# Kernel tuning notes

Hardware: AMD Instinct MI355X
Metric: run time of the kernel (lower is better)

Reference implementation:

```python
import jax, jax.numpy as jnp
import numpy as np
import math

B, NX, NY = 4, 64, 64
IN_DIM, OUT_DIM = 3, 3
DIM, DEPTH, HEADS, DH, FF_MULT = 192, 6, 8, 64, 4
INNER = HEADS * DH              # 512
FF = DIM * FF_MULT              # 768
M = int(DH * math.log(DH))      # 266 random features (performer default)
GROUPS = 8
LATENT_STEPS = 1
EPS_SN, EPS_K, EPS_GN = 1e-5, 1e-4, 1e-5


def setup_inputs() -> dict:
    rng = np.random.default_rng(0)
    f = lambda *s: jnp.asarray(rng.standard_normal(s).astype(np.float32) * 0.02)
    # unitary forward operator (SVD-whitened in torch == orthogonal matrix)
    Q, _ = np.linalg.qr(rng.standard_normal((DIM, DIM)).astype(np.float32))
    return {
        "x": jnp.asarray(rng.standard_normal((B, NX, NY, IN_DIM)).astype(np.float32)),
        "to_in_w": f(DIM, IN_DIM), "to_in_b": f(DIM),
        "pos_emb": f(1, NX * NY, DIM),
        "proj": jnp.asarray(rng.standard_normal((DEPTH, M, DH)).astype(np.float32)),
        "sn_attn_g": jnp.ones((DEPTH,), jnp.float32),
        "wq": f(DEPTH, INNER, DIM), "wk": f(DEPTH, INNER, DIM), "wv": f(DEPTH, INNER, DIM),
        "wo": f(DEPTH, DIM, INNER), "bo": f(DEPTH, DIM),
        "sn_ff_g": jnp.ones((DEPTH,), jnp.float32),
        "w1": f(DEPTH, FF, DIM), "b1": f(DEPTH, FF),
        "w2": f(DEPTH, DIM, FF), "b2": f(DEPTH, DIM),
        "expand_w": f(DIM, DIM),
        "fwd_w": jnp.asarray(Q.astype(np.float32)),
        "dec_lin_w": f(DIM, DIM), "dec_lin_b": f(DIM),
        "gn_g": jnp.ones((DIM,), jnp.float32), "gn_b": jnp.zeros((DIM,), jnp.float32),
        "c9_w": f(DIM, DIM // GROUPS, 9, 9), "c9_b": f(DIM),
        "c7_w": f(DIM // 2, DIM // GROUPS, 7, 7), "c7_b": f(DIM // 2),
        "c5_w": f(DIM // 4, (DIM // 2) // GROUPS, 5, 5), "c5_b": f(DIM // 4),
        "c1_w": f(OUT_DIM, DIM // 4, 1, 1), "c1_b": f(OUT_DIM),
        "latent_steps": LATENT_STEPS,
    }


def _scalenorm(x, g):
    n = jnp.linalg.norm(x, axis=-1, keepdims=True) * (x.shape[-1] ** -0.5)
    return x / jnp.maximum(n, EPS_SN) * g


def _softmax_features(data, proj, is_query):
    # data: [b,h,n,d]; proj: [m,d] -> FAVOR+ softmax-kernel features [b,h,n,m]
    dn = data.shape[-1] ** -0.25
    ratio = proj.shape[0] ** -0.5
    dd = jnp.einsum('bhnd,md->bhnm', data * dn, proj)
    diag = 0.5 * jnp.sum(data * data, -1) * (dn * dn)  # [b,h,n]
    if is_query:
        mx = jnp.max(dd, axis=-1, keepdims=True)
    else:
        mx = jnp.max(dd, axis=(-1, -2), keepdims=True)
    return ratio * (jnp.exp(dd - diag[..., None] - mx) + EPS_K)


def _attn(x, proj, wq, wk, wv, wo, bo):
    b, n, _ = x.shape
    split = lambda t: t.reshape(b, n, HEADS, DH).transpose(0, 2, 1, 3)
    q = split(x @ wq.T); k = split(x @ wk.T); v = split(x @ wv.T)
    qp = _softmax_features(q, proj, True)
    kp = _softmax_features(k, proj, False)
    context = jnp.einsum('bhnm,bhnd->bhmd', kp, v)            # [b,h,m,d]
    denom = jnp.einsum('bhnm,bhm->bhn', qp, kp.sum(2))
    out = jnp.einsum('bhnm,bhmd->bhnd', qp, context) / denom[..., None]
    out = out.transpose(0, 2, 1, 3).reshape(b, n, INNER)
    return out @ wo.T + bo


def _circ_conv(x, w, b, groups):
    p = w.shape[-1] // 2
    x = jnp.pad(x, ((0, 0), (0, 0), (p, p), (p, p)), mode='wrap')
    y = jax.lax.conv_general_dilated(x, w, (1, 1), 'VALID',
        dimension_numbers=('NCHW', 'OIHW', 'NCHW'), feature_group_count=groups)
    return y + b[None, :, None, None]


def _group_norm(x, g, b):
    B_, C, H, W = x.shape
    xg = x.reshape(B_, GROUPS, C // GROUPS, H, W)
    mu = xg.mean((2, 3, 4), keepdims=True)
    var = xg.var((2, 3, 4), keepdims=True)
    xn = ((xg - mu) * jax.lax.rsqrt(var + EPS_GN)).reshape(B_, C, H, W)
    return xn * g[None, :, None, None] + b[None, :, None, None]


def reference(x, to_in_w, to_in_b, pos_emb, proj, sn_attn_g, wq, wk, wv, wo, bo,
              sn_ff_g, w1, b1, w2, b2, expand_w, fwd_w, dec_lin_w, dec_lin_b,
              gn_g, gn_b, c9_w, c9_b, c7_w, c7_b, c5_w, c5_b, c1_w, c1_b, latent_steps):
    b, nx, ny, _ = x.shape
    h = x @ to_in_w.T + to_in_b                       # [b,nx,ny,dim]
    h = h.reshape(b, nx * ny, DIM) + pos_emb[:, :nx * ny]
    for i in range(DEPTH):                             # Performer: prenorm attn + prenorm FF
        h = h + _attn(_scalenorm(h, sn_attn_g[i]), proj[i], wq[i], wk[i], wv[i], wo[i], bo[i])
        hn = _scalenorm(h, sn_ff_g[i])
        h = h + (jax.nn.gelu(hn @ w1[i].T + b1[i], approximate=False) @ w2[i].T + b2[i])
    h = h.reshape(b, nx, ny, DIM) @ expand_w.T        # expand_latent (no bias)
    u, us = h, []
    for _ in range(latent_steps):
        u = u @ fwd_w.T                               # unitary forward operator
        us.append(u)
    u = jnp.concatenate(us, 0)                        # [(b*t), nx, ny, c]
    y = u @ dec_lin_w.T + dec_lin_b
    y = y.transpose(0, 3, 1, 2)                       # NCHW
    y = _group_norm(y, gn_g, gn_b)
    y = jax.nn.gelu(_circ_conv(y, c9_w, c9_b, GROUPS), approximate=False)
    y = jax.nn.gelu(_circ_conv(y, c7_w, c7_b, GROUPS), approximate=False)
    y = jax.nn.gelu(_circ_conv(y, c5_w, c5_b, GROUPS), approximate=False)
    y = jax.lax.conv_general_dilated(y, c1_w, (1, 1), 'VALID',
        dimension_numbers=('NCHW', 'OIHW', 'NCHW')) + c1_b[None, :, None, None]
    # einops '(b t) c nx ny -> b t nx ny c'
    y = y.reshape(b, latent_steps, OUT_DIM, nx, ny).transpose(0, 1, 3, 4, 2)
    return y
```

## Files before the change

### kernel.cpp

```cpp
#include <hip/hip_runtime.h>
#include <cmath>

#define NB      4
#define NTOK    4096
#define BNTOK   16384
#define CDIM    192
#define CINNER  512
#define NHEADS  8
#define DHEAD   64
#define CFF     768
#define MFEAT   266
#define NDEPTH  6

#define DN      0.35355339059327373f
#define RATIO   0.06131393394849658f

typedef unsigned short u16;
typedef __attribute__((ext_vector_type(8))) short s16x8;
typedef __attribute__((ext_vector_type(8))) u16  u16x8;
typedef __attribute__((ext_vector_type(4))) float f32x4;

#define OFF_H    0ull
#define OFF_HN   3145728ull
#define OFF_Q    6291456ull
#define OFF_K    14680064ull
#define OFF_V    23068672ull
#define OFF_BIG  31457280ull
#define OFF_PJ   44040192ull
#define OFF_CTXT 44163072ull
#define OFF_KMAX 47368192ull
#define OFF_GNP  47368448ull
#define OFF_GNS  47369472ull
#define OFF_WHI  47370240ull
#define OFF_WLO  49489920ull
#define WOFF_QKV 0ull
#define WOFF_WO  1769472ull
#define WOFF_W1  2359296ull
#define WOFF_W2  3244032ull
#define WOFF_EXP 4128768ull
#define WOFF_FWD 4165632ull
#define WOFF_DEC 4202496ull

#define PJL      20480
#define CTXTN    819200

__device__ __forceinline__ float gelu_f(float x) {
    return 0.5f * x * (1.0f + erff(x * 0.7071067811865476f));
}
__device__ __forceinline__ unsigned f2ord(float f) {
    int i = __float_as_int(f);
    return (i >= 0) ? ((unsigned)i | 0x80000000u) : (unsigned)(~i);
}
__device__ __forceinline__ float ord2f(unsigned u) {
    int i = (u & 0x80000000u) ? (int)(u & 0x7fffffffu) : ~(int)u;
    return __int_as_float(i);
}
__device__ __forceinline__ void split_bf16(float a, u16& h, u16& l) {
    unsigned ua = __float_as_uint(a);
    unsigned rh = (ua + 0x7FFFu + ((ua >> 16) & 1u)) >> 16;
    h = (u16)rh;
    float hf = __uint_as_float(rh << 16);
    float lo = a - hf;
    unsigned ul = __float_as_uint(lo);
    unsigned rl = (ul + 0x7FFFu + ((ul >> 16) & 1u)) >> 16;
    l = (u16)rl;
}
__device__ __forceinline__ u16 hi_bf16(float a) {
    unsigned ua = __float_as_uint(a);
    return (u16)((ua + 0x7FFFu + ((ua >> 16) & 1u)) >> 16);
}

__global__ __launch_bounds__(256) void cvt_qkv(const float* __restrict__ wq,
    const float* __restrict__ wk, const float* __restrict__ wv,
    u16* __restrict__ hi, u16* __restrict__ lo)
{
    int idx = blockIdx.x * 256 + threadIdx.x;
    int l = idx / 294912, rem = idx - l * 294912;
    int r = rem / 192, c = rem - r * 192;
    float v;
    if (r < 512)       v = wq[((size_t)l * 512 + r) * 192 + c];
    else if (r < 1024) v = wk[((size_t)l * 512 + (r - 512)) * 192 + c];
    else               v = wv[((size_t)l * 512 + (r - 1024)) * 192 + c];
    u16 h, lw; split_bf16(v, h, lw);
    hi[idx] = h; lo[idx] = lw;
}

__global__ __launch_bounds__(256) void cvt_w(const float* __restrict__ src,
    u16* __restrict__ hi, u16* __restrict__ lo, int n)
{
    int idx = blockIdx.x * 256 + threadIdx.x;
    if (idx < n) {
        u16 h, l; split_bf16(src[idx], h, l);
        hi[idx] = h; lo[idx] = l;
    }
}

__global__ __launch_bounds__(256) void cvt_dec(const float* __restrict__ e,
    const float* __restrict__ f, const float* __restrict__ d,
    u16* __restrict__ hi, u16* __restrict__ lo)
{
    int idx = blockIdx.x * 256 + threadIdx.x;
    if (idx >= 110592) return;
    int which = idx / 36864, rem = idx - which * 36864;
    float v = (which == 0) ? e[rem] : (which == 1) ? f[rem] : d[rem];
    u16 h, l; split_bf16(v, h, l);
    hi[idx] = h; lo[idx] = l;
}

__global__ __launch_bounds__(256) void cvt_pj(const float* __restrict__ proj,
    u16* __restrict__ hi, u16* __restrict__ lo)
{
    int idx = blockIdx.x * 256 + threadIdx.x;
    int l = idx / PJL, rem = idx - l * PJL;
    int m = rem >> 6, k = rem & 63;
    float v = (m < MFEAT) ? proj[(size_t)l * MFEAT * DHEAD + m * 64 + k] : 0.f;
    u16 h, lw; split_bf16(v, h, lw);
    hi[idx] = h; lo[idx] = lw;
}

__global__ __launch_bounds__(256) void input_embed(const float* __restrict__ x,
    const float* __restrict__ w, const float* __restrict__ bvec,
    const float* __restrict__ pos, float* __restrict__ h)
{
    int idx = blockIdx.x * 256 + threadIdx.x;
    int row = idx / CDIM, c = idx - row * CDIM;
    int p = row & (NTOK - 1);
    const float* xr = x + (size_t)row * 3;
    h[idx] = xr[0]*w[c*3+0] + xr[1]*w[c*3+1] + xr[2]*w[c*3+2] + bvec[c] + pos[(size_t)p*CDIM + c];
}

__global__ __launch_bounds__(256) void rownorm_kernel(const float* __restrict__ in,
    float* __restrict__ sv, const float* __restrict__ gptr, int gidx)
{
    int wv = threadIdx.x >> 6, lane = threadIdx.x & 63;
    int row = blockIdx.x * 4 + wv;
    const float* p = in + (size_t)row * CDIM;
    float x0 = p[lane], x1 = p[lane + 64], x2 = p[lane + 128];
    float ss = x0*x0 + x1*x1 + x2*x2;
    #pragma unroll
    for (int off = 32; off; off >>= 1) ss += __shfl_xor(ss, off);
    if (lane == 0) {
        float g = gptr[gidx];
        float n = sqrtf(ss * (1.0f / 192.0f));
        sv[row] = g / fmaxf(n, 1e-5f);
    }
}

#define LP 40
__global__ __launch_bounds__(256) void gemm_mfma(const float* __restrict__ A,
    const float* __restrict__ ascale,
    const u16* __restrict__ Bhi, const u16* __restrict__ Blo,
    const float* __restrict__ bias, const float* __restrict__ resid,
    float* __restrict__ C, int M, int N, int K, int epi)
{
    __shared__ u16 a_hi[128 * LP], a_lo[128 * LP], b_hi[128 * LP], b_lo[128 * LP];
    const int tid = threadIdx.x;
    const int n0 = blockIdx.x * 128, m0 = blockIdx.y * 128;
    const int wave = tid >> 6, lane = tid & 63;
    const int wr = wave >> 1, wc = wave & 1;
    const int fr = lane & 15, q = lane >> 4;
    const bool wactive = (n0 + wc * 64) < N;
    f32x4 acc[4][4];
    #pragma unroll
    for (int i = 0; i < 4; ++i)
        #pragma unroll
        for (int j = 0; j < 4; ++j) { acc[i][j][0]=0.f; acc[i][j][1]=0.f; acc[i][j][2]=0.f; acc[i][j][3]=0.f; }

    const int srow = tid >> 1, sc0 = (tid & 1) * 16;
    const float* aptr = A + (size_t)(m0 + srow) * K + sc0;
    const float as = ascale ? ascale[m0 + srow] : 1.0f;
    const bool bval = (n0 + srow) < N;
    const u16* bhp = Bhi + (size_t)(n0 + srow) * K + sc0;
    const u16* blp = Blo + (size_t)(n0 + srow) * K + sc0;
    const int soff = srow * LP + sc0;
    const int aoffb = (wr * 64 + fr) * LP + q * 8;
    const int boffb = (wc * 64 + fr) * LP + q * 8;

    for (int kc = 0; kc < K; kc += 32) {
        float4 f0 = *(const float4*)(aptr + kc);
        float4 f1 = *(const float4*)(aptr + kc + 4);
        float4 f2 = *(const float4*)(aptr + kc + 8);
        float4 f3 = *(const float4*)(aptr + kc + 12);
        u16x8 h0, l0, h1, l1;
        {
            float v[16] = {f0.x,f0.y,f0.z,f0.w, f1.x,f1.y,f1.z,f1.w,
                           f2.x,f2.y,f2.z,f2.w, f3.x,f3.y,f3.z,f3.w};
            u16 hh[16], ll[16];
            #pragma unroll
            for (int i = 0; i < 16; ++i) { float sv = v[i] * as; split_bf16(sv, hh[i], ll[i]); }
            #pragma unroll
            for (int i = 0; i < 8; ++i) { h0[i]=hh[i]; l0[i]=ll[i]; h1[i]=hh[8+i]; l1[i]=ll[8+i]; }
        }
        *(u16x8*)&a_hi[soff]     = h0;  *(u16x8*)&a_hi[soff + 8] = h1;
        *(u16x8*)&a_lo[soff]     = l0;  *(u16x8*)&a_lo[soff + 8] = l1;
        u16x8 bh0 = (u16x8)0, bh1 = (u16x8)0, bl0 = (u16x8)0, bl1 = (u16x8)0;
        if (bval) {
            bh0 = *(const u16x8*)(bhp + kc);  bh1 = *(const u16x8*)(bhp + kc + 8);
            bl0 = *(const u16x8*)(blp + kc);  bl1 = *(const u16x8*)(blp + kc + 8);
        }
        *(u16x8*)&b_hi[soff]     = bh0;  *(u16x8*)&b_hi[soff + 8] = bh1;
        *(u16x8*)&b_lo[soff]     = bl0;  *(u16x8*)&b_lo[soff + 8] = bl1;
        __syncthreads();
        if (wactive) {
            s16x8 Ah[4], Al[4], Bh[4], Bl[4];
            #pragma unroll
            for (int t = 0; t < 4; ++t) {
                Ah[t] = *(const s16x8*)&a_hi[aoffb + t * 16 * LP];
                Al[t] = *(const s16x8*)&a_lo[aoffb + t * 16 * LP];
                Bh[t] = *(const s16x8*)&b_hi[boffb + t * 16 * LP];
                Bl[t] = *(const s16x8*)&b_lo[boffb + t * 16 * LP];
            }
            #pragma unroll
            for (int i = 0; i < 4; ++i)
                #pragma unroll
                for (int j = 0; j < 4; ++j)
                    acc[i][j] = __builtin_amdgcn_mfma_f32_16x16x32_bf16(Ah[i], Bh[j], acc[i][j], 0, 0, 0);
            #pragma unroll
            for (int i = 0; i < 4; ++i)
                #pragma unroll
                for (int j = 0; j < 4; ++j)
                    acc[i][j] = __builtin_amdgcn_mfma_f32_16x16x32_bf16(Ah[i], Bl[j], acc[i][j], 0, 0, 0);
            #pragma unroll
            for (int i = 0; i < 4; ++i)
                #pragma unroll
                for (int j = 0; j < 4; ++j)
                    acc[i][j] = __builtin_amdgcn_mfma_f32_16x16x32_bf16(Al[i], Bh[j], acc[i][j], 0, 0, 0);
        }
        __syncthreads();
    }
    const int c0 = n0 + wc * 64;
    const int rowb = m0 + wr * 64;
    #pragma unroll
    for (int j = 0; j < 4; ++j) {
        int c = c0 + j * 16 + fr;
        if (c >= N) continue;
        float bb = (epi & 1) ? bias[c] : 0.f;
        float* cp;
        if (epi & 8) cp = C + (size_t)(c >> 9) * 8388608ull + (size_t)(c & 511);
        else         cp = C + c;
        const float* rp = (epi & 4) ? (resid + c) : nullptr;
        #pragma unroll
        for (int i = 0; i < 4; ++i) {
            #pragma unroll
            for (int r = 0; r < 4; ++r) {
                int row = rowb + i * 16 + q * 4 + r;
                float val = acc[i][j][r] + bb;
                if (epi & 2) val = gelu_f(val);
                if (epi & 4) val += rp[(size_t)row * N];
                size_t off = (epi & 8) ? (size_t)row * 512 : (size_t)row * N;
                cp[off] = val;
            }
        }
    }
}

__global__ void kmax_init(unsigned* kmaxu) {
    if (threadIdx.x < NDEPTH * 32) kmaxu[threadIdx.x] = 0u;
}

__global__ __launch_bounds__(256) void kmax2_kernel(const float* __restrict__ Km,
    const u16* __restrict__ pjh, unsigned* __restrict__ kmaxu)
{
    __shared__ __align__(16) u16 khi[64 * 72];
    __shared__ float wred[4];
    const int tid = threadIdx.x;
    const int nt = blockIdx.x, bh = blockIdx.y;
    const int b = bh >> 3, hh = bh & 7;
    const int wave = tid >> 6, lane = tid & 63;
    const int fr = lane & 15, quad = lane >> 4;
    float lm = -1e30f;
    const size_t kbase = ((size_t)b * NTOK) * CINNER + hh * DHEAD;
    for (int ch = 0; ch < 4; ++ch) {
        const int n0 = nt * 256 + ch * 64;
        __syncthreads();
        {
            int tok = tid >> 2, koff = (tid & 3) * 16;
            const float* kp = Km + kbase + (size_t)(n0 + tok) * CINNER + koff;
            u16 hh16[16];
            #pragma unroll
            for (int qd = 0; qd < 4; ++qd) {
                float4 f = *(const float4*)(kp + qd * 4);
                hh16[qd*4+0] = hi_bf16(f.x * DN); hh16[qd*4+1] = hi_bf16(f.y * DN);
                hh16[qd*4+2] = hi_bf16(f.z * DN); hh16[qd*4+3] = hi_bf16(f.w * DN);
            }
            u16x8 v0, v1;
            #pragma unroll
            for (int i = 0; i < 8; ++i) { v0[i] = hh16[i]; v1[i] = hh16[8+i]; }
            *(u16x8*)&khi[tok * 72 + koff] = v0;
            *(u16x8*)&khi[tok * 72 + koff + 8] = v1;
        }
        __syncthreads();
        int rowA = (wave * 16 + fr) * 72;
        s16x8 A0 = *(const s16x8*)&khi[rowA + quad * 8];
        s16x8 A1 = *(const s16x8*)&khi[rowA + 32 + quad * 8];
        for (int ct = 0; ct < 17; ++ct) {
            const u16* bp = pjh + (ct * 16 + fr) * 64 + quad * 8;
            s16x8 B0 = *(const s16x8*)bp;
            s16x8 B1 = *(const s16x8*)(bp + 32);
            f32x4 t; t[0]=0.f; t[1]=0.f; t[2]=0.f; t[3]=0.f;
            t = __builtin_amdgcn_mfma_f32_16x16x32_bf16(A0, B0, t, 0, 0, 0);
            t = __builtin_amdgcn_mfma_f32_16x16x32_bf16(A1, B1, t, 0, 0, 0);
            if (ct * 16 + fr < MFEAT) {
                #pragma unroll
                for (int r = 0; r < 4; ++r) lm = fmaxf(lm, t[r]);
            }
        }
    }
    #pragma unroll
    for (int off = 32; off; off >>= 1) lm = fmaxf(lm, __shfl_xor(lm, off));
    if (lane == 0) wred[wave] = lm;
    __syncthreads();
    if (tid == 0) {
        float m = fmaxf(fmaxf(wred[0], wred[1]), fmaxf(wred[2], wred[3]));
        atomicMax(kmaxu + bh, f2ord(m));
    }
}

__global__ __launch_bounds__(256) void ctx2_kernel(const float* __restrict__ Km,
    const float* __restrict__ Vm, const u16* __restrict__ pjh, const u16* __restrict__ pjl,
    const unsigned* __restrict__ kmaxu, float* __restrict__ part)
{
    __shared__ __align__(16) u16 khi[32 * 72], klo[32 * 72];
    __shared__ __align__(16) u16 vth[80 * 40], vtl[80 * 40];
    __shared__ __align__(16) u16 kph[4][16 * 40], kpl[4][16 * 40];
    __shared__ float diag[32];
    const int tid = threadIdx.x;
    const int bh = blockIdx.x, seg = blockIdx.y;
    const int b = bh >> 3, hh = bh & 7;
    const int wave = tid >> 6, lane = tid & 63;
    const int fr = lane & 15, quad = lane >> 4;
    const float kmx = ord2f(kmaxu[bh]);
    for (int i = tid; i < 16 * 40; i += 256) {
        int row = 64 + i / 40, col = i - (i / 40) * 40;
        vth[row * 40 + col] = (row == 64) ? (u16)0x3F80 : (u16)0;
        vtl[row * 40 + col] = 0;
    }
    f32x4 accv[5][5];
    #pragma unroll
    for (int i = 0; i < 5; ++i)
        #pragma unroll
        for (int j = 0; j < 5; ++j) { accv[i][j][0]=0.f; accv[i][j][1]=0.f; accv[i][j][2]=0.f; accv[i][j][3]=0.f; }
    const size_t rowbase = ((size_t)b * NTOK) * CINNER + hh * DHEAD;
    u16* sh = kph[wave];  u16* sl = kpl[wave];
    for (int nc = 0; nc < 16; ++nc) {
        const int n0 = seg * 512 + nc * 32;
        __syncthreads();
        {
            int tok = tid >> 3, koff = (tid & 7) * 8;
            const float* kp = Km + rowbase + (size_t)(n0 + tok) * CINNER + koff;
            float4 f0 = *(const float4*)kp;
            float4 f1 = *(const float4*)(kp + 4);
            float v[8] = {f0.x*DN, f0.y*DN, f0.z*DN, f0.w*DN, f1.x*DN, f1.y*DN, f1.z*DN, f1.w*DN};
            u16x8 hv, lv; float ps = 0.f;
            #pragma unroll
            for (int i = 0; i < 8; ++i) { u16 h, l; split_bf16(v[i], h, l); hv[i]=h; lv[i]=l; ps += v[i]*v[i]; }
            *(u16x8*)&khi[tok * 72 + koff] = hv;
            *(u16x8*)&klo[tok * 72 + koff] = lv;
            ps += __shfl_xor(ps, 1); ps += __shfl_xor(ps, 2); ps += __shfl_xor(ps, 4);
            if ((tid & 7) == 0) diag[tok] = 0.5f * ps;
            const float* vp = Vm + rowbase + (size_t)(n0 + tok) * CINNER + koff;
            float4 g0 = *(const float4*)vp;
            float4 g1 = *(const float4*)(vp + 4);
            float vv[8] = {g0.x, g0.y, g0.z, g0.w, g1.x, g1.y, g1.z, g1.w};
            #pragma unroll
            for (int i = 0; i < 8; ++i) {
                u16 h, l; split_bf16(vv[i], h, l);
                vth[(koff + i) * 40 + tok] = h;
                vtl[(koff + i) * 40 + tok] = l;
            }
        }
        __syncthreads();
        s16x8 Ah[2][2], Al[2][2];
        #pragma unroll
        for (int rt = 0; rt < 2; ++rt) {
            int rowA = (rt * 16 + fr) * 72;
            Ah[rt][0] = *(const s16x8*)&khi[rowA + quad * 8];
            Ah[rt][1] = *(const s16x8*)&khi[rowA + 32 + quad * 8];
            Al[rt][0] = *(const s16x8*)&klo[rowA + quad * 8];
            Al[rt][1] = *(const s16x8*)&klo[rowA + 32 + quad * 8];
        }
        for (int mc = 0; mc < 5; ++mc) {
            const int ct = mc * 4 + wave;
            const u16* bph = pjh + (ct * 16 + fr) * 64 + quad * 8;
            const u16* bpl = pjl + (ct * 16 + fr) * 64 + quad * 8;
            s16x8 B0h = *(const s16x8*)bph, B1h = *(const s16x8*)(bph + 32);
            s16x8 B0l = *(const s16x8*)bpl, B1l = *(const s16x8*)(bpl + 32);
            const bool valid = (ct * 16 + fr) < MFEAT;
            #pragma unroll
            for (int rt = 0; rt < 2; ++rt) {
                f32x4 dd; dd[0]=0.f; dd[1]=0.f; dd[2]=0.f; dd[3]=0.f;
                dd = __builtin_amdgcn_mfma_f32_16x16x32_bf16(Ah[rt][0], B0h, dd, 0, 0, 0);
                dd = __builtin_amdgcn_mfma_f32_16x16x32_bf16(Ah[rt][0], B0l, dd, 0, 0, 0);
                dd = __builtin_amdgcn_mfma_f32_16x16x32_bf16(Al[rt][0], B0h, dd, 0, 0, 0);
                dd = __builtin_amdgcn_mfma_f32_16x16x32_bf16(Ah[rt][1], B1h, dd, 0, 0, 0);
                dd = __builtin_amdgcn_mfma_f32_16x16x32_bf16(Ah[rt][1], B1l, dd, 0, 0, 0);
                dd = __builtin_amdgcn_mfma_f32_16x16x32_bf16(Al[rt][1], B1h, dd, 0, 0, 0);
                ushort4 ph, pl;
                #pragma unroll
                for (int r = 0; r < 4; ++r) {
                    float dgv = diag[rt * 16 + quad * 4 + r];
                    float val = valid ? RATIO * (expf(dd[r] - dgv - kmx) + 1e-4f) : 0.f;
                    u16 h, l; split_bf16(val, h, l);
                    (&ph.x)[r] = h; (&pl.x)[r] = l;
                }
                *(ushort4*)&sh[fr * 40 + rt * 16 + quad * 4] = ph;
                *(ushort4*)&sl[fr * 40 + rt * 16 + quad * 4] = pl;
            }
            s16x8 Bh = *(const s16x8*)&sh[fr * 40 + quad * 8];
            s16x8 Bl = *(const s16x8*)&sl[fr * 40 + quad * 8];
            #pragma unroll
            for (int rt2 = 0; rt2 < 5; ++rt2) {
                s16x8 Vh = *(const s16x8*)&vth[(rt2 * 16 + fr) * 40 + quad * 8];
                s16x8 Vl = *(const s16x8*)&vtl[(rt2 * 16 + fr) * 40 + quad * 8];
                accv[rt2][mc] = __builtin_amdgcn_mfma_f32_16x16x32_bf16(Vh, Bh, accv[rt2][mc], 0, 0, 0);
                accv[rt2][mc] = __builtin_amdgcn_mfma_f32_16x16x32_bf16(Vh, Bl, accv[rt2][mc], 0, 0, 0);
                accv[rt2][mc] = __builtin_amdgcn_mfma_f32_16x16x32_bf16(Vl, Bh, accv[rt2][mc], 0, 0, 0);
            }
        }
    }
    float* pb = part + ((size_t)(seg * 32 + bh)) * 80 * 320;
    #pragma unroll
    for (int rt2 = 0; rt2 < 5; ++rt2) {
        #pragma unroll
        for (int mc = 0; mc < 5; ++mc) {
            int ct = mc * 4 + wave;
            #pragma unroll
            for (int r = 0; r < 4; ++r)
                pb[(size_t)(rt2 * 16 + quad * 4 + r) * 320 + ct * 16 + fr] = accv[rt2][mc][r];
        }
    }
}

__global__ __launch_bounds__(256) void ctxt_reduce(const float* __restrict__ part,
    u16* __restrict__ cth, u16* __restrict__ ctl)
{
    int idx = blockIdx.x * 256 + threadIdx.x;
    float s = 0.f;
    #pragma unroll
    for (int sg = 0; sg < 8; ++sg) s += part[(size_t)sg * CTXTN + idx];
    u16 h, l; split_bf16(s, h, l);
    cth[idx] = h; ctl[idx] = l;
}

__global__ __launch_bounds__(256) void qside2_kernel(const float* __restrict__ Qm,
    const u16* __restrict__ pjh, const u16* __restrict__ pjl,
    const u16* __restrict__ cth, const u16* __restrict__ ctl,
    float* __restrict__ attn_out)
{
    __shared__ __align__(16) u16 qhi[64 * 72], qlo[64 * 72];
    __shared__ __align__(16) u16 slabh[4][16 * 72], slabl[4][16 * 72];
    __shared__ float diag[64];
    const int tid = threadIdx.x;
    const int nt = blockIdx.x, bh = blockIdx.y;
    const int b = bh >> 3, hh = bh & 7;
    const int wave = tid >> 6, lane = tid & 63;
    const int fr = lane & 15, quad = lane >> 4;
    const int n0 = nt * 64;
    {
        int tok = tid >> 2, koff = (tid & 3) * 16;
        const float* qp = Qm + ((size_t)(b * NTOK + n0 + tok)) * CINNER + hh * DHEAD + koff;
        float v[16]; float ps = 0.f;
        #pragma unroll
        for (int qd = 0; qd < 4; ++qd) {
            float4 f = *(const float4*)(qp + qd * 4);
            v[qd*4+0]=f.x*DN; v[qd*4+1]=f.y*DN; v[qd*4+2]=f.z*DN; v[qd*4+3]=f.w*DN;
        }
        u16x8 h0, l0, h1, l1;
        #pragma unroll
        for (int i = 0; i < 8; ++i) {
            u16 h, l; split_bf16(v[i], h, l); h0[i]=h; l0[i]=l;
            split_bf16(v[8+i], h, l); h1[i]=h; l1[i]=l;
        }
        #pragma unroll
        for (int i = 0; i < 16; ++i) ps += v[i]*v[i];
        *(u16x8*)&qhi[tok * 72 + koff] = h0;  *(u16x8*)&qhi[tok * 72 + koff + 8] = h1;
        *(u16x8*)&qlo[tok * 72 + koff] = l0;  *(u16x8*)&qlo[tok * 72 + koff + 8] = l1;
        ps += __shfl_xor(ps, 1); ps += __shfl_xor(ps, 2);
        if ((tid & 3) == 0) diag[tok] = 0.5f * ps;
    }
    __syncthreads();
    f32x4 dd[20];
    #pragma unroll
    for (int ct = 0; ct < 20; ++ct) { dd[ct][0]=0.f; dd[ct][1]=0.f; dd[ct][2]=0.f; dd[ct][3]=0.f; }
    {
        int rowA = (wave * 16 + fr) * 72;
        s16x8 A0h = *(const s16x8*)&qhi[rowA + quad * 8];
        s16x8 A1h = *(const s16x8*)&qhi[rowA + 32 + quad * 8];
        s16x8 A0l = *(const s16x8*)&qlo[rowA + quad * 8];
        s16x8 A1l = *(const s16x8*)&qlo[rowA + 32 + quad * 8];
        #pragma unroll
        for (int ct = 0; ct < 20; ++ct) {
            const u16* bph = pjh + (ct * 16 + fr) * 64 + quad * 8;
            const u16* bpl = pjl + (ct * 16 + fr) * 64 + quad * 8;
            s16x8 B0h = *(const s16x8*)bph, B1h = *(const s16x8*)(bph + 32);
            s16x8 B0l = *(const s16x8*)bpl, B1l = *(const s16x8*)(bpl + 32);
            dd[ct] = __builtin_amdgcn_mfma_f32_16x16x32_bf16(A0h, B0h, dd[ct], 0, 0, 0);
            dd[ct] = __builtin_amdgcn_mfma_f32_16x16x32_bf16(A0h, B0l, dd[ct], 0, 0, 0);
            dd[ct] = __builtin_amdgcn_mfma_f32_16x16x32_bf16(A0l, B0h, dd[ct], 0, 0, 0);
            dd[ct] = __builtin_amdgcn_mfma_f32_16x16x32_bf16(A1h, B1h, dd[ct], 0, 0, 0);
            dd[ct] = __builtin_amdgcn_mfma_f32_16x16x32_bf16(A1h, B1l, dd[ct], 0, 0, 0);
            dd[ct] = __builtin_amdgcn_mfma_f32_16x16x32_bf16(A1l, B1h, dd[ct], 0, 0, 0);
        }
    }
    float pm[4] = {-1e30f, -1e30f, -1e30f, -1e30f};
    #pragma unroll
    for (int ct = 0; ct < 20; ++ct) {
        if (ct * 16 + fr < MFEAT) {
            #pragma unroll
            for (int r = 0; r < 4; ++r) pm[r] = fmaxf(pm[r], dd[ct][r]);
        }
    }
    #pragma unroll
    for (int r = 0; r < 4; ++r) {
        pm[r] = fmaxf(pm[r], __shfl_xor(pm[r], 1));
        pm[r] = fmaxf(pm[r], __shfl_xor(pm[r], 2));
        pm[r] = fmaxf(pm[r], __shfl_xor(pm[r], 4));
        pm[r] = fmaxf(pm[r], __shfl_xor(pm[r], 8));
    }
    float dg[4];
    #pragma unroll
    for (int r = 0; r < 4; ++r) dg[r] = diag[wave * 16 + quad * 4 + r];
    #pragma unroll
    for (int ct = 0; ct < 20; ++ct) {
        bool valid = (ct * 16 + fr) < MFEAT;
        #pragma unroll
        for (int r = 0; r < 4; ++r)
            dd[ct][r] = valid ? RATIO * (expf(dd[ct][r] - dg[r] - pm[r]) + 1e-4f) : 0.f;
    }
    f32x4 acc[5];
    #pragma unroll
    for (int dt = 0; dt < 5; ++dt) { acc[dt][0]=0.f; acc[dt][1]=0.f; acc[dt][2]=0.f; acc[dt][3]=0.f; }
    u16* sh = slabh[wave];  u16* sl = slabl[wave];
    for (int mc = 0; mc < 5; ++mc) {
        #pragma unroll
        for (int c = 0; c < 4; ++c) {
            int ct = mc * 4 + c;
            #pragma unroll
            for (int r = 0; r < 4; ++r) {
                u16 h, l; split_bf16(dd[ct][r], h, l);
                int tok = quad * 4 + r;
                sh[tok * 72 + c * 16 + fr] = h;
                sl[tok * 72 + c * 16 + fr] = l;
            }
        }
        #pragma unroll
        for (int ks = 0; ks < 2; ++ks) {
            s16x8 Ah = *(const s16x8*)&sh[fr * 72 + ks * 32 + quad * 8];
            s16x8 Al = *(const s16x8*)&sl[fr * 72 + ks * 32 + quad * 8];
            #pragma unroll
            for (int dt = 0; dt < 5; ++dt) {
                const u16* bph = cth + ((size_t)bh * 80 + dt * 16 + fr) * 320 + mc * 64 + ks * 32 + quad * 8;
                const u16* bpl = ctl + ((size_t)bh * 80 + dt * 16 + fr) * 320 + mc * 64 + ks * 32 + quad * 8;
                s16x8 Bh = *(const s16x8*)bph;
                s16x8 Bl = *(const s16x8*)bpl;
                acc[dt] = __builtin_amdgcn_mfma_f32_16x16x32_bf16(Ah, Bh, acc[dt], 0, 0, 0);
                acc[dt] = __builtin_amdgcn_mfma_f32_16x16x32_bf16(Ah, Bl, acc[dt], 0, 0, 0);
                acc[dt] = __builtin_amdgcn_mfma_f32_16x16x32_bf16(Al, Bh, acc[dt], 0, 0, 0);
            }
        }
    }
    #pragma unroll
    for (int r = 0; r < 4; ++r) {
        float denom = __shfl(acc[4][r], lane & 48);
        float inv = 1.0f / denom;
        int token = n0 + wave * 16 + quad * 4 + r;
        float* op = attn_out + ((size_t)(b * NTOK + token)) * CINNER + hh * DHEAD;
        #pragma unroll
        for (int dt = 0; dt < 4; ++dt)
            op[dt * 16 + fr] = acc[dt][r] * inv;
    }
}

__global__ __launch_bounds__(256) void gn_part_kernel(const float* __restrict__ y,
    float2* __restrict__ part)
{
    __shared__ float s_s[256], s_q[256];
    const int tid = threadIdx.x;
    const int sp = blockIdx.x, g = blockIdx.y, b = blockIdx.z;
    int p = sp * 256 + tid;
    const float* base = y + ((size_t)(b * NTOK + p)) * CDIM + g * 24;
    float s = 0.f, q = 0.f;
    #pragma unroll
    for (int i = 0; i < 24; ++i) { float v = base[i]; s += v; q += v * v; }
    s_s[tid] = s; s_q[tid] = q;
    __syncthreads();
    for (int st = 128; st; st >>= 1) {
        if (tid < st) { s_s[tid] += s_s[tid + st]; s_q[tid] += s_q[tid + st]; }
        __syncthreads();
    }
    if (tid == 0) part[(b * 8 + g) * 16 + sp] = make_float2(s_s[0], s_q[0]);
}

__global__ void gn_stat_kernel(const float2* __restrict__ part, float2* __restrict__ stat)
{
    int bg = threadIdx.x;
    if (bg < 32) {
        float s = 0.f, q = 0.f;
        for (int i = 0; i < 16; ++i) { float2 v = part[bg * 16 + i]; s += v.x; q += v.y; }
        float mean = s * (1.0f / 98304.0f);
        float var = q * (1.0f / 98304.0f) - mean * mean;
        stat[bg] = make_float2(mean, rsqrtf(var + 1e-5f));
    }
}

__global__ __launch_bounds__(256) void gn_apply_kernel(const float* __restrict__ y,
    const float2* __restrict__ stat, const float* __restrict__ gg,
    const float* __restrict__ gb, float* __restrict__ out)
{
    __shared__ float tile[64][65];
    const int tid = threadIdx.x;
    const int pt = blockIdx.x, ct = blockIdx.y, b = blockIdx.z;
    const int p0 = pt * 64, c0 = ct * 64;
    #pragma unroll
    for (int r = 0; r < 4; ++r) {
        int id = tid + r * 256;
        int pr = id >> 4, kq = (id & 15) * 4;
        float4 v = *(const float4*)(y + ((size_t)(b * NTOK + p0 + pr)) * CDIM + c0 + kq);
        tile[pr][kq+0] = v.x; tile[pr][kq+1] = v.y; tile[pr][kq+2] = v.z; tile[pr][kq+3] = v.w;
    }
    __syncthreads();
    const int cc = tid >> 6, pp = tid & 63;
    #pragma unroll
    for (int i = 0; i < 16; ++i) {
        int c = c0 + cc * 16 + i;
        int g = c / 24;
        float2 st = stat[b * 8 + g];
        float v = tile[pp][cc * 16 + i];
        out[((size_t)(b * CDIM + c)) * NTOK + p0 + pp] = (v - st.x) * st.y * gg[c] + gb[c];
    }
}

template<int KS, int CIN, int COUT, int OX, int YS, int OCB>
__global__ __launch_bounds__(256) void circ_conv3(const float* __restrict__ in,
    const float* __restrict__ w, const float* __restrict__ bias,
    float* __restrict__ out, int do_gelu)
{
    constexpr int P   = KS / 2;
    constexpr int ICG = CIN / 8;
    constexpr int OCG = COUT / 8;
    constexpr int TW  = 64 + 2 * P;
    constexpr int TR  = 64 / YS + 2 * P;
    constexpr int RS0 = (TW + 3) & ~3;
    constexpr int RS  = (RS0 % 8 == 0) ? RS0 + 4 : RS0;
    constexpr int TCX = 64 / OX;
    constexpr int RV  = (OX + KS - 1 + 3) & ~3;
    constexpr int NLD = (TR * TW + 255) / 256;
    __shared__ __align__(16) float tile[TR * RS];
    const int tid = threadIdx.x;
    const int oc0 = blockIdx.x * OCB;
    const int y0  = blockIdx.y * (64 / YS);
    const int b   = blockIdx.z;
    const int g   = oc0 / OCG;
    const int tx  = tid % TCX, ty = tid / TCX;
    int srcs[NLD], dsts[NLD];
    #pragma unroll
    for (int j = 0; j < NLD; ++j) {
        int idx = tid + j * 256;
        if (idx < TR * TW) {
            int r = idx / TW, c = idx - r * TW;
            int gy = (y0 + r - P) & 63, gx = (c - P) & 63;
            srcs[j] = gy * 64 + gx;
            dsts[j] = r * RS + c;
        } else { srcs[j] = 0; dsts[j] = -1; }
    }
    float acc[OCB][OX] = {};
    const float* ip0 = in + ((size_t)(b * CIN + g * ICG)) * 4096;
    #pragma unroll 1
    for (int ic = 0; ic < ICG; ++ic) {
        __syncthreads();
        const float* ip = ip0 + (size_t)ic * 4096;
        #pragma unroll
        for (int j = 0; j < NLD; ++j)
            if (dsts[j] >= 0) tile[dsts[j]] = ip[srcs[j]];
        __syncthreads();
        const float* wp = w + ((size_t)oc0 * ICG + ic) * (KS * KS);
        #pragma unroll 1
        for (int ky = 0; ky < KS; ++ky) {
            float wreg[OCB][KS];
            #pragma unroll
            for (int oc = 0; oc < OCB; ++oc)
                #pragma unroll
                for (int kx = 0; kx < KS; ++kx)
                    wreg[oc][kx] = wp[(size_t)oc * ICG * KS * KS + ky * KS + kx];
            float rv[RV];
            const float* rp = &tile[(ty + ky) * RS + tx * OX];
            #pragma unroll
            for (int q2 = 0; q2 < RV / 4; ++q2)
                *(float4*)&rv[q2 * 4] = *(const float4*)(rp + q2 * 4);
            #pragma unroll
            for (int kx = 0; kx < KS; ++kx)
                #pragma unroll
                for (int oc = 0; oc < OCB; ++oc)
                    #pragma unroll
                    for (int ox = 0; ox < OX; ++ox)
                        acc[oc][ox] += rv[kx + ox] * wreg[oc][kx];
        }
    }
    const int y = y0 + ty, x = tx * OX;
    #pragma unroll
    for (int oc = 0; oc < OCB; ++oc) {
        float bv = bias[oc0 + oc];
        float vo[OX];
        #pragma unroll
        for (int ox = 0; ox < OX; ++ox) {
            float vv = acc[oc][ox] + bv;
            vo[ox] = do_gelu ? gelu_f(vv) : vv;
        }
        float* op = out + (((size_t)(b * COUT + oc0 + oc) * 64 + y)) * 64 + x;
        #pragma unroll
        for (int q2 = 0; q2 < OX / 4; ++q2)
            *(float4*)(op + q2 * 4) = *(float4*)&vo[q2 * 4];
    }
}

__global__ __launch_bounds__(256) void conv1_kernel(const float* __restrict__ in,
    const float* __restrict__ w, const float* __restrict__ bias, float* __restrict__ out)
{
    int idx = blockIdx.x * 256 + threadIdx.x;
    int b = idx >> 12, p = idx & 4095;
    float a0 = bias[0], a1 = bias[1], a2 = bias[2];
    const float* ip = in + (size_t)b * 48 * NTOK + p;
    #pragma unroll 8
    for (int ic = 0; ic < 48; ++ic) {
        float v = ip[(size_t)ic * NTOK];
        a0 += v * w[ic]; a1 += v * w[48 + ic]; a2 += v * w[96 + ic];
    }
    float* op = out + (size_t)idx * 3;
    op[0] = a0; op[1] = a1; op[2] = a2;
}

static inline void gemm_mf(hipStream_t s, const float* A, const float* ascale,
                           const u16* Bhi, const u16* Blo,
                           const float* bias, const float* resid, float* C,
                           int M, int N, int K, int epi)
{
    dim3 g((N + 127) / 128, M / 128);
    hipLaunchKernelGGL(gemm_mfma, g, dim3(256), 0, s, A, ascale, Bhi, Blo, bias, resid, C, M, N, K, epi);
}

extern "C" void kernel_launch(void* const* d_in, const int* in_sizes, int n_in,
                              void* d_out, int out_size, void* d_ws, size_t ws_size,
                              hipStream_t stream)
{
    (void)in_sizes; (void)n_in; (void)out_size; (void)ws_size;
    const float* x        = (const float*)d_in[0];
    const float* to_in_w  = (const float*)d_in[1];
    const float* to_in_b  = (const float*)d_in[2];
    const float* pos_emb  = (const float*)d_in[3];
    const float* proj     = (const float*)d_in[4];
    const float* sn_attn_g= (const float*)d_in[5];
    const float* wq       = (const float*)d_in[6];
    const float* wk       = (const float*)d_in[7];
    const float* wv       = (const float*)d_in[8];
    const float* wo       = (const float*)d_in[9];
    const float* bo       = (const float*)d_in[10];
    const float* sn_ff_g  = (const float*)d_in[11];
    const float* w1       = (const float*)d_in[12];
    const float* b1       = (const float*)d_in[13];
    const float* w2       = (const float*)d_in[14];
    const float* b2       = (const float*)d_in[15];
    const float* expand_w = (const float*)d_in[16];
    const float* fwd_w    = (const float*)d_in[17];
    const float* dec_lin_w= (const float*)d_in[18];
    const float* dec_lin_b= (const float*)d_in[19];
    const float* gn_g     = (const float*)d_in[20];
    const float* gn_b     = (const float*)d_in[21];
    const float* c9_w     = (const float*)d_in[22];
    const float* c9_b     = (const float*)d_in[23];
    const float* c7_w     = (const float*)d_in[24];
    const float* c7_b     = (const float*)d_in[25];
    const float* c5_w     = (const float*)d_in[26];
    const float* c5_b     = (const float*)d_in[27];
    const float* c1_w     = (const float*)d_in[28];
    const float* c1_b     = (const float*)d_in[29];
    float* out = (float*)d_out;

    float* ws = (float*)d_ws;
    float* h   = ws + OFF_H;
    float* hn  = ws + OFF_HN;
    float* sbuf = ws + OFF_HN;
    float* q   = ws + OFF_Q;
    float* k   = ws + OFF_K;
    float* v   = ws + OFF_V;
    float* big = ws + OFF_BIG;
    u16* pjhi = (u16*)(ws + OFF_PJ);
    u16* pjlo = pjhi + 6 * PJL;
    u16* cthi = (u16*)(ws + OFF_CTXT);
    u16* ctlo = cthi + CTXTN;
    unsigned* kmaxu = (unsigned*)(ws + OFF_KMAX);
    float2* gnp = (float2*)(ws + OFF_GNP);
    float2* gns = (float2*)(ws + OFF_GNS);
    u16* whi = (u16*)(ws + OFF_WHI);
    u16* wlo = (u16*)(ws + OFF_WLO);

    hipLaunchKernelGGL(input_embed, dim3(BNTOK * CDIM / 256), dim3(256), 0, stream,
                       x, to_in_w, to_in_b, pos_emb, h);
    hipLaunchKernelGGL(kmax_init, dim3(1), dim3(256), 0, stream, kmaxu);
    hipLaunchKernelGGL(cvt_qkv, dim3(6912), dim3(256), 0, stream, wq, wk, wv,
                       whi + WOFF_QKV, wlo + WOFF_QKV);
    hipLaunchKernelGGL(cvt_w, dim3(2304), dim3(256), 0, stream, wo, whi + WOFF_WO, wlo + WOFF_WO, 589824);
    hipLaunchKernelGGL(cvt_w, dim3(3456), dim3(256), 0, stream, w1, whi + WOFF_W1, wlo + WOFF_W1, 884736);
    hipLaunchKernelGGL(cvt_w, dim3(3456), dim3(256), 0, stream, w2, whi + WOFF_W2, wlo + WOFF_W2, 884736);
    hipLaunchKernelGGL(cvt_dec, dim3(432), dim3(256), 0, stream, expand_w, fwd_w, dec_lin_w,
                       whi + WOFF_EXP, wlo + WOFF_EXP);
    hipLaunchKernelGGL(cvt_pj, dim3(480), dim3(256), 0, stream, proj, pjhi, pjlo);

    for (int l = 0; l < NDEPTH; ++l) {
        const float* bo_l = bo + (size_t)l * CDIM;
        const float* b1_l = b1 + (size_t)l * CFF;
        const float* b2_l = b2 + (size_t)l * CDIM;
        const u16* pjh_l = pjhi + (size_t)l * PJL;
        const u16* pjl_l = pjlo + (size_t)l * PJL;
        unsigned* kmax_l = kmaxu + l * 32;

        hipLaunchKernelGGL(rownorm_kernel, dim3(BNTOK / 4), dim3(256), 0, stream, h, sbuf, sn_attn_g, l);
        gemm_mf(stream, h, sbuf, whi + WOFF_QKV + (size_t)l * 294912, wlo + WOFF_QKV + (size_t)l * 294912,
                nullptr, nullptr, q, BNTOK, 1536, CDIM, 8);
        hipLaunchKernelGGL(kmax2_kernel, dim3(16, 32), dim3(256), 0, stream, k, pjh_l, kmax_l);
        hipLaunchKernelGGL(ctx2_kernel, dim3(32, 8), dim3(256), 0, stream, k, v, pjh_l, pjl_l, kmax_l, big);
        hipLaunchKernelGGL(ctxt_reduce, dim3(CTXTN / 256), dim3(256), 0, stream, big, cthi, ctlo);
        hipLaunchKernelGGL(qside2_kernel, dim3(64, 32), dim3(256), 0, stream, q, pjh_l, pjl_l, cthi, ctlo, k);
        gemm_mf(stream, k, nullptr, whi + WOFF_WO + (size_t)l * 98304, wlo + WOFF_WO + (size_t)l * 98304,
                bo_l, h, h, BNTOK, CDIM, CINNER, 1 | 4);

        hipLaunchKernelGGL(rownorm_kernel, dim3(BNTOK / 4), dim3(256), 0, stream, h, sbuf, sn_ff_g, l);
        gemm_mf(stream, h, sbuf, whi + WOFF_W1 + (size_t)l * 147456, wlo + WOFF_W1 + (size_t)l * 147456,
                b1_l, nullptr, big, BNTOK, CFF, CDIM, 1 | 2);
        gemm_mf(stream, big, nullptr, whi + WOFF_W2 + (size_t)l * 147456, wlo + WOFF_W2 + (size_t)l * 147456,
                b2_l, h, h, BNTOK, CDIM, CFF, 1 | 4);
    }

    gemm_mf(stream, h, nullptr, whi + WOFF_EXP, wlo + WOFF_EXP, nullptr, nullptr, hn, BNTOK, CDIM, CDIM, 0);
    gemm_mf(stream, hn, nullptr, whi + WOFF_FWD, wlo + WOFF_FWD, nullptr, nullptr, h, BNTOK, CDIM, CDIM, 0);
    gemm_mf(stream, h, nullptr, whi + WOFF_DEC, wlo + WOFF_DEC, dec_lin_b, nullptr, hn, BNTOK, CDIM, CDIM, 1);

    float* y0 = big;
    float* y1 = big + 3145728;
    float* y2 = big + 6291456;
    float* y3 = big + 7864320;
    hipLaunchKernelGGL(gn_part_kernel, dim3(16, 8, 4), dim3(256), 0, stream, hn, gnp);
    hipLaunchKernelGGL(gn_stat_kernel, dim3(1), dim3(32), 0, stream, gnp, gns);
    hipLaunchKernelGGL(gn_apply_kernel, dim3(64, 3, 4), dim3(256), 0, stream, hn, gns, gn_g, gn_b, y0);

    hipLaunchKernelGGL((circ_conv3<9, 192, 192, 8, 2, 3>), dim3(64, 2, 4), dim3(256), 0, stream,
                       y0, c9_w, c9_b, y1, 1);
    hipLaunchKernelGGL((circ_conv3<7, 192, 96, 8, 2, 3>), dim3(32, 2, 4), dim3(256), 0, stream,
                       y1, c7_w, c7_b, y2, 1);
    hipLaunchKernelGGL((circ_conv3<5, 96, 48, 4, 4, 3>), dim3(16, 4, 4), dim3(256), 0, stream,
                       y2, c5_w, c5_b, y3, 1);
    hipLaunchKernelGGL(conv1_kernel, dim3(BNTOK / 256), dim3(256), 0, stream, y3, c1_w, c1_b, out);
}
```

Measured before the change: 3.613 ms.

## Split context accumulation finer, double-buffer conv input channels, shrink conv OC blocks

```diff
diff --git a/kernel.cpp b/kernel.cpp
--- a/kernel.cpp
+++ b/kernel.cpp
@@ -42,7 +42,8 @@
 #define WOFF_DEC 4202496ull
 
 #define PJL      20480
-#define CTXTN    819200
+#define NSEG     16
+#define CTXP     20800
 
 __device__ __forceinline__ float gelu_f(float x) {
     return 0.5f * x * (1.0f + erff(x * 0.7071067811865476f));
@@ -342,8 +343,8 @@
         for (int j = 0; j < 5; ++j) { accv[i][j][0]=0.f; accv[i][j][1]=0.f; accv[i][j][2]=0.f; accv[i][j][3]=0.f; }
     const size_t rowbase = ((size_t)b * NTOK) * CINNER + hh * DHEAD;
     u16* sh = kph[wave];  u16* sl = kpl[wave];
-    for (int nc = 0; nc < 16; ++nc) {
-        const int n0 = seg * 512 + nc * 32;
+    for (int nc = 0; nc < 8; ++nc) {
+        const int n0 = seg * 256 + nc * 32;
         __syncthreads();
         {
             int tok = tid >> 3, koff = (tid & 7) * 8;
@@ -418,15 +419,18 @@
             }
         }
     }
-    float* pb = part + ((size_t)(seg * 32 + bh)) * 80 * 320;
+    float* pb = part + ((size_t)(seg * 32 + bh)) * CTXP;
     #pragma unroll
     for (int rt2 = 0; rt2 < 5; ++rt2) {
         #pragma unroll
         for (int mc = 0; mc < 5; ++mc) {
             int ct = mc * 4 + wave;
             #pragma unroll
-            for (int r = 0; r < 4; ++r)
-                pb[(size_t)(rt2 * 16 + quad * 4 + r) * 320 + ct * 16 + fr] = accv[rt2][mc][r];
+            for (int r = 0; r < 4; ++r) {
+                int row = rt2 * 16 + quad * 4 + r;
+                if (row < 65)
+                    pb[(size_t)row * 320 + ct * 16 + fr] = accv[rt2][mc][r];
+            }
         }
     }
 }
@@ -435,11 +439,15 @@
     u16* __restrict__ cth, u16* __restrict__ ctl)
 {
     int idx = blockIdx.x * 256 + threadIdx.x;
+    if (idx >= 32 * CTXP) return;
     float s = 0.f;
     #pragma unroll
-    for (int sg = 0; sg < 8; ++sg) s += part[(size_t)sg * CTXTN + idx];
+    for (int sg = 0; sg < NSEG; ++sg) s += part[(size_t)sg * 32 * CTXP + idx];
+    int bh = idx / CTXP, rem = idx - bh * CTXP;
+    int row = rem / 320, col = rem - row * 320;
     u16 h, l; split_bf16(s, h, l);
-    cth[idx] = h; ctl[idx] = l;
+    size_t o = ((size_t)bh * 80 + row) * 320 + col;
+    cth[o] = h; ctl[o] = l;
 }
 
 __global__ __launch_bounds__(256) void qside2_kernel(const float* __restrict__ Qm,
@@ -631,7 +639,7 @@
 }
 
 template<int KS, int CIN, int COUT, int OX, int YS, int OCB>
-__global__ __launch_bounds__(256) void circ_conv3(const float* __restrict__ in,
+__global__ __launch_bounds__(256) void circ_conv4(const float* __restrict__ in,
     const float* __restrict__ w, const float* __restrict__ bias,
     float* __restrict__ out, int do_gelu)
 {
@@ -645,7 +653,7 @@
     constexpr int TCX = 64 / OX;
     constexpr int RV  = (OX + KS - 1 + 3) & ~3;
     constexpr int NLD = (TR * TW + 255) / 256;
-    __shared__ __align__(16) float tile[TR * RS];
+    __shared__ __align__(16) float tile[2][TR * RS];
     const int tid = threadIdx.x;
     const int oc0 = blockIdx.x * OCB;
     const int y0  = blockIdx.y * (64 / YS);
@@ -666,34 +674,42 @@
     float acc[OCB][OX] = {};
     const float* ip0 = in + ((size_t)(b * CIN + g * ICG)) * 4096;
     #pragma unroll 1
-    for (int ic = 0; ic < ICG; ++ic) {
+    for (int ic = 0; ic < ICG; ic += 2) {
         __syncthreads();
-        const float* ip = ip0 + (size_t)ic * 4096;
+        const float* ipa = ip0 + (size_t)ic * 4096;
+        const float* ipb = ipa + 4096;
         #pragma unroll
         for (int j = 0; j < NLD; ++j)
-            if (dsts[j] >= 0) tile[dsts[j]] = ip[srcs[j]];
+            if (dsts[j] >= 0) {
+                tile[0][dsts[j]] = ipa[srcs[j]];
+                tile[1][dsts[j]] = ipb[srcs[j]];
+            }
         __syncthreads();
-        const float* wp = w + ((size_t)oc0 * ICG + ic) * (KS * KS);
         #pragma unroll 1
-        for (int ky = 0; ky < KS; ++ky) {
-            float wreg[OCB][KS];
-            #pragma unroll
-            for (int oc = 0; oc < OCB; ++oc)
-                #pragma unroll
-                for (int kx = 0; kx < KS; ++kx)
-                    wreg[oc][kx] = wp[(size_t)oc * ICG * KS * KS + ky * KS + kx];
-            float rv[RV];
-            const float* rp = &tile[(ty + ky) * RS + tx * OX];
-            #pragma unroll
-            for (int q2 = 0; q2 < RV / 4; ++q2)
-                *(float4*)&rv[q2 * 4] = *(const float4*)(rp + q2 * 4);
-            #pragma unroll
-            for (int kx = 0; kx < KS; ++kx)
+        for (int pp = 0; pp < 2; ++pp) {
+            const float* wp = w + ((size_t)oc0 * ICG + ic + pp) * (KS * KS);
+            const float* tp = tile[pp];
+            #pragma unroll 1
+            for (int ky = 0; ky < KS; ++ky) {
+                float wreg[OCB][KS];
                 #pragma unroll
                 for (int oc = 0; oc < OCB; ++oc)
                     #pragma unroll
-                    for (int ox = 0; ox < OX; ++ox)
-                        acc[oc][ox] += rv[kx + ox] * wreg[oc][kx];
+                    for (int kx = 0; kx < KS; ++kx)
+                        wreg[oc][kx] = wp[(size_t)oc * ICG * KS * KS + ky * KS + kx];
+                float rv[RV];
+                const float* rp = &tp[(ty + ky) * RS + tx * OX];
+                #pragma unroll
+                for (int q2 = 0; q2 < RV / 4; ++q2)
+                    *(float4*)&rv[q2 * 4] = *(const float4*)(rp + q2 * 4);
+                #pragma unroll
+                for (int kx = 0; kx < KS; ++kx)
+                    #pragma unroll
+                    for (int oc = 0; oc < OCB; ++oc)
+                        #pragma unroll
+                        for (int ox = 0; ox < OX; ++ox)
+                            acc[oc][ox] += rv[kx + ox] * wreg[oc][kx];
+            }
         }
     }
     const int y = y0 + ty, x = tx * OX;
@@ -786,7 +802,7 @@
     u16* pjhi = (u16*)(ws + OFF_PJ);
     u16* pjlo = pjhi + 6 * PJL;
     u16* cthi = (u16*)(ws + OFF_CTXT);
-    u16* ctlo = cthi + CTXTN;
+    u16* ctlo = cthi + 32 * 80 * 320;
     unsigned* kmaxu = (unsigned*)(ws + OFF_KMAX);
     float2* gnp = (float2*)(ws + OFF_GNP);
     float2* gns = (float2*)(ws + OFF_GNS);
@@ -815,17 +831,17 @@
 
         hipLaunchKernelGGL(rownorm_kernel, dim3(BNTOK / 4), dim3(256), 0, stream, h, sbuf, sn_attn_g, l);
         gemm_mf(stream, h, sbuf, whi + WOFF_QKV + (size_t)l * 294912, wlo + WOFF_QKV + (size_t)l * 294912,
-                nullptr, nullptr, q, BNTOK, 1536, CDIM, 8);
+                nullptr, nullptr, q, BNTOK, 1536, CDIM, 8 | 16);
         hipLaunchKernelGGL(kmax2_kernel, dim3(16, 32), dim3(256), 0, stream, k, pjh_l, kmax_l);
-        hipLaunchKernelGGL(ctx2_kernel, dim3(32, 8), dim3(256), 0, stream, k, v, pjh_l, pjl_l, kmax_l, big);
-        hipLaunchKernelGGL(ctxt_reduce, dim3(CTXTN / 256), dim3(256), 0, stream, big, cthi, ctlo);
+        hipLaunchKernelGGL(ctx2_kernel, dim3(32, NSEG), dim3(256), 0, stream, k, v, pjh_l, pjl_l, kmax_l, big);
+        hipLaunchKernelGGL(ctxt_reduce, dim3((32 * CTXP + 255) / 256), dim3(256), 0, stream, big, cthi, ctlo);
         hipLaunchKernelGGL(qside2_kernel, dim3(64, 32), dim3(256), 0, stream, q, pjh_l, pjl_l, cthi, ctlo, k);
         gemm_mf(stream, k, nullptr, whi + WOFF_WO + (size_t)l * 98304, wlo + WOFF_WO + (size_t)l * 98304,
                 bo_l, h, h, BNTOK, CDIM, CINNER, 1 | 4);
 
         hipLaunchKernelGGL(rownorm_kernel, dim3(BNTOK / 4), dim3(256), 0, stream, h, sbuf, sn_ff_g, l);
         gemm_mf(stream, h, sbuf, whi + WOFF_W1 + (size_t)l * 147456, wlo + WOFF_W1 + (size_t)l * 147456,
-                b1_l, nullptr, big, BNTOK, CFF, CDIM, 1 | 2);
+                b1_l, nullptr, big, BNTOK, CFF, CDIM, 1 | 2 | 16);
         gemm_mf(stream, big, nullptr, whi + WOFF_W2 + (size_t)l * 147456, wlo + WOFF_W2 + (size_t)l * 147456,
                 b2_l, h, h, BNTOK, CDIM, CFF, 1 | 4);
     }
@@ -842,11 +858,11 @@
     hipLaunchKernelGGL(gn_stat_kernel, dim3(1), dim3(32), 0, stream, gnp, gns);
     hipLaunchKernelGGL(gn_apply_kernel, dim3(64, 3, 4), dim3(256), 0, stream, hn, gns, gn_g, gn_b, y0);
 
-    hipLaunchKernelGGL((circ_conv3<9, 192, 192, 8, 2, 3>), dim3(64, 2, 4), dim3(256), 0, stream,
+    hipLaunchKernelGGL((circ_conv4<9, 192, 192, 8, 2, 2>), dim3(96, 2, 4), dim3(256), 0, stream,
                        y0, c9_w, c9_b, y1, 1);
-    hipLaunchKernelGGL((circ_conv3<7, 192, 96, 8, 2, 3>), dim3(32, 2, 4), dim3(256), 0, stream,
+    hipLaunchKernelGGL((circ_conv4<7, 192, 96, 8, 2, 2>), dim3(48, 2, 4), dim3(256), 0, stream,
                        y1, c7_w, c7_b, y2, 1);
-    hipLaunchKernelGGL((circ_conv3<5, 96, 48, 4, 4, 3>), dim3(16, 4, 4), dim3(256), 0, stream,
+    hipLaunchKernelGGL((circ_conv4<5, 96, 48, 4, 4, 2>), dim3(24, 4, 4), dim3(256), 0, stream,
                        y2, c5_w, c5_b, y3, 1);
     hipLaunchKernelGGL(conv1_kernel, dim3(BNTOK / 256), dim3(256), 0, stream, y3, c1_w, c1_b, out);
 }
```

Result: no change. 3.574 ms (-1.1%).
